# Kernel optimization log

Measured on AMD Instinct MI355X. Metric: run time of the kernel, lower is better.

## Reference

```python
import jax, jax.numpy as jnp
import numpy as np

N_Q, N_T, D, C = 4096, 8192, 512, 16
SIGMA = 2.0


def setup_inputs() -> dict:
    key = jax.random.key(0)
    k1, k2, k3 = jax.random.split(key, 3)
    X = jax.random.normal(k1, (N_Q, D), dtype=jnp.float32)
    X_train = jax.random.normal(k2, (N_T, D), dtype=jnp.float32)
    y = jax.random.randint(k3, (N_T,), 0, C, dtype=jnp.int32)
    sigma = jnp.float32(SIGMA)
    return {"X": X, "X_train": X_train, "y": y, "sigma": sigma}


def reference(X, X_train, y, sigma):
    xx = jnp.sum(X * X, axis=1, keepdims=True)              # [N_q, 1]
    tt = jnp.sum(X_train * X_train, axis=1)                 # [N_t]
    cross = jnp.einsum('qd,td->qt', X, X_train)             # [N_q, N_t]
    dist2 = jnp.maximum(xx + tt[None, :] - 2.0 * cross, 0.0)
    pattern = jnp.exp(-dist2 / (2.0 * sigma ** 2))          # Gaussian RBF kernel [N_q, N_t]
    # per-class segment sum over training patterns (replaces per-class Python loop)
    summation = jax.ops.segment_sum(pattern.T, y, num_segments=C).T  # [N_q, C]
    summation = summation / jnp.sum(summation, axis=1, keepdims=True)
    return jnp.argmax(summation, axis=1)
```

## Files before the change

kernel.cpp:

```cpp
#include <hip/hip_runtime.h>


#define NQ 4096
#define NT 8192
#define DD 512
#define NC 16
#define BM 256
#define BN 256
#define BK 64
#define NKT (DD / BK)
#define LN_FLT_MIN -87.336544750402f
#define SCREEN_T 706.0f

typedef __attribute__((ext_vector_type(8))) short bf16x8;
typedef __attribute__((ext_vector_type(4))) float f32x4;
typedef __attribute__((ext_vector_type(8))) unsigned short u16x8;

static __device__ __forceinline__ unsigned short f2bf(float f) {
  unsigned u = __float_as_uint(f);
  u = u + 0x7FFFu + ((u >> 16) & 1u);
  return (unsigned short)(u >> 16);
}

__global__ __launch_bounds__(256) void prep_k(const float* __restrict__ X,
                                              const float* __restrict__ XT,
                                              unsigned short* __restrict__ bX,
                                              unsigned short* __restrict__ bT,
                                              float* __restrict__ xx,
                                              float* __restrict__ tt,
                                              float* __restrict__ classacc) {
  const int lane = threadIdx.x & 63;
  const int row  = blockIdx.x * 4 + (threadIdx.x >> 6);
  const float* src; unsigned short* dst; float* nrm;
  if (row < NT) { src = XT + (size_t)row * DD; dst = bT + (size_t)row * DD; nrm = tt + row; }
  else { const int r = row - NT; src = X + (size_t)r * DD; dst = bX + (size_t)r * DD; nrm = xx + r; }
  const float4* s4 = (const float4*)src;
  const float4 a = s4[lane * 2], b = s4[lane * 2 + 1];
  u16x8 o;
  o[0] = f2bf(a.x); o[1] = f2bf(a.y); o[2] = f2bf(a.z); o[3] = f2bf(a.w);
  o[4] = f2bf(b.x); o[5] = f2bf(b.y); o[6] = f2bf(b.z); o[7] = f2bf(b.w);
  *((u16x8*)dst + lane) = o;
  float acc = a.x*a.x + a.y*a.y + a.z*a.z + a.w*a.w
            + b.x*b.x + b.y*b.y + b.z*b.z + b.w*b.w;
  #pragma unroll
  for (int off = 32; off; off >>= 1) acc += __shfl_down(acc, off, 64);
  if (lane == 0) *nrm = acc;
  if (blockIdx.x < 64) {
    float4 z = {0.f, 0.f, 0.f, 0.f};
    ((float4*)classacc)[blockIdx.x * 256 + threadIdx.x] = z;
  }
}

static __device__ __forceinline__ void stage_unit(const unsigned short* __restrict__ src,
                                                  int rowbase, int colbyte,
                                                  char* unitbase, int tid) {
  #pragma unroll
  for (int i = 0; i < 2; ++i) {
    const int row = i * 128 + (tid >> 2);
    const int sl  = (tid & 3) ^ ((row >> 1) & 3);
    const char* gp = (const char*)(src + (size_t)(rowbase + row) * DD) + colbyte + sl * 16;
    __builtin_amdgcn_global_load_lds(
        (const __attribute__((address_space(1))) unsigned int*)gp,
        (__attribute__((address_space(3))) unsigned int*)(unitbase + i * 8192 + (tid >> 6) * 1024),
        16, 0, 0);
  }
}

#define BAR() __builtin_amdgcn_s_barrier()

__global__ __launch_bounds__(512, 2) void pnn_mfma(const unsigned short* __restrict__ bX,
                                                   const unsigned short* __restrict__ bT,
                                                   const float* __restrict__ Xf,
                                                   const float* __restrict__ Tf,
                                                   const int* __restrict__ y,
                                                   const float* __restrict__ sigp,
                                                   const float* __restrict__ xx,
                                                   const float* __restrict__ tt,
                                                   float* __restrict__ classacc) {
  extern __shared__ char lds[];
  const int tid  = threadIdx.x;
  const int w    = tid >> 6, lane = tid & 63;
  const int wr   = w >> 2, wc = w & 3;
  const int lo   = lane & 15, hi = lane >> 4;

  const int bid = blockIdx.x;
  const int xcd = bid & 7, c = bid >> 3;
  const int qt = (xcd & 1) * 8 + (c >> 3);
  const int tn = (xcd >> 1) * 8 + (c & 7);
  const int qbase = qt * BM, tbase = tn * BN;

  char* const A0 = lds;
  char* const A1 = lds + 32768;
  char* const B0 = lds + 65536;
  char* const B1 = lds + 98304;

  const int sfix = (hi ^ ((lo >> 1) & 3)) * 16;
  const int aoff = (wr * 128 + lo) * 64 + sfix;
  const int boff = (wc * 64 + lo) * 64 + sfix;

  stage_unit(bX, qbase, 0,  A0,         tid);
  stage_unit(bT, tbase, 0,  B0,         tid);
  stage_unit(bX, qbase, 64, A0 + 16384, tid);
  stage_unit(bT, tbase, 64, B0 + 16384, tid);
  asm volatile("s_waitcnt vmcnt(4)" ::: "memory");
  __builtin_amdgcn_sched_barrier(0);
  BAR();

  f32x4 acc[8][4];
  #pragma unroll
  for (int m = 0; m < 8; ++m)
    #pragma unroll
    for (int n = 0; n < 4; ++n) acc[m][n] = (f32x4)(0.0f);

  char* Ac = A0; char* Bc = B0; char* An = A1; char* Bn = B1;

  for (int kt = 0; kt < NKT; ++kt) {
    const bool more = (kt < NKT - 1);
    const int nk = (kt + 1) * 128;
    bf16x8 a[8], b0, b1;

    #pragma unroll
    for (int m = 0; m < 8; ++m) a[m] = *(const bf16x8*)(Ac + m * 1024 + aoff);
    b0 = *(const bf16x8*)(Bc + 0 * 1024 + boff);
    b1 = *(const bf16x8*)(Bc + 1 * 1024 + boff);
    if (more) stage_unit(bX, qbase, nk, An, tid);
    BAR();
    __builtin_amdgcn_s_setprio(1);
    #pragma unroll
    for (int m = 0; m < 8; ++m) {
      acc[m][0] = __builtin_amdgcn_mfma_f32_16x16x32_bf16(a[m], b0, acc[m][0], 0, 0, 0);
      acc[m][1] = __builtin_amdgcn_mfma_f32_16x16x32_bf16(a[m], b1, acc[m][1], 0, 0, 0);
    }
    __builtin_amdgcn_s_setprio(0);
    BAR();

    b0 = *(const bf16x8*)(Bc + 2 * 1024 + boff);
    b1 = *(const bf16x8*)(Bc + 3 * 1024 + boff);
    if (more) stage_unit(bT, tbase, nk, Bn, tid);
    BAR();
    __builtin_amdgcn_s_setprio(1);
    #pragma unroll
    for (int m = 0; m < 8; ++m) {
      acc[m][2] = __builtin_amdgcn_mfma_f32_16x16x32_bf16(a[m], b0, acc[m][2], 0, 0, 0);
      acc[m][3] = __builtin_amdgcn_mfma_f32_16x16x32_bf16(a[m], b1, acc[m][3], 0, 0, 0);
    }
    __builtin_amdgcn_s_setprio(0);
    if (more) asm volatile("s_waitcnt vmcnt(4)" ::: "memory");
    else      asm volatile("s_waitcnt vmcnt(0)" ::: "memory");
    BAR();

    #pragma unroll
    for (int m = 0; m < 8; ++m) a[m] = *(const bf16x8*)(Ac + 16384 + m * 1024 + aoff);
    b0 = *(const bf16x8*)(Bc + 16384 + 0 * 1024 + boff);
    b1 = *(const bf16x8*)(Bc + 16384 + 1 * 1024 + boff);
    if (more) stage_unit(bX, qbase, nk + 64, An + 16384, tid);
    BAR();
    __builtin_amdgcn_s_setprio(1);
    #pragma unroll
    for (int m = 0; m < 8; ++m) {
      acc[m][0] = __builtin_amdgcn_mfma_f32_16x16x32_bf16(a[m], b0, acc[m][0], 0, 0, 0);
      acc[m][1] = __builtin_amdgcn_mfma_f32_16x16x32_bf16(a[m], b1, acc[m][1], 0, 0, 0);
    }
    __builtin_amdgcn_s_setprio(0);
    BAR();

    b0 = *(const bf16x8*)(Bc + 16384 + 2 * 1024 + boff);
    b1 = *(const bf16x8*)(Bc + 16384 + 3 * 1024 + boff);
    if (more) stage_unit(bT, tbase, nk + 64, Bn + 16384, tid);
    BAR();
    __builtin_amdgcn_s_setprio(1);
    #pragma unroll
    for (int m = 0; m < 8; ++m) {
      acc[m][2] = __builtin_amdgcn_mfma_f32_16x16x32_bf16(a[m], b0, acc[m][2], 0, 0, 0);
      acc[m][3] = __builtin_amdgcn_mfma_f32_16x16x32_bf16(a[m], b1, acc[m][3], 0, 0, 0);
    }
    __builtin_amdgcn_s_setprio(0);
    if (more) asm volatile("s_waitcnt vmcnt(4)" ::: "memory");
    BAR();

    char* t0 = Ac; Ac = An; An = t0;
    char* t1 = Bc; Bc = Bn; Bn = t1;
  }

  const float sg = sigp[0];
  const float inv2s2 = 1.0f / (2.0f * sg * sg);
  const int qb = qbase + wr * 128;
  const int tb = tbase + wc * 64;
  float tnorm[4]; int tcls[4];
  #pragma unroll
  for (int n = 0; n < 4; ++n) {
    const int t = tb + n * 16 + lo;
    tnorm[n] = tt[t]; tcls[n] = y[t];
  }
  #pragma unroll
  for (int m = 0; m < 8; ++m) {
    #pragma unroll
    for (int r = 0; r < 4; ++r) {
      const int q = qb + m * 16 + hi * 4 + r;
      const float xq = xx[q];
      #pragma unroll
      for (int n = 0; n < 4; ++n) {
        const float d2 = xq + tnorm[n] - 2.0f * acc[m][n][r];
        if (__builtin_expect(d2 < SCREEN_T, 0)) {
          const int t = tb + n * 16 + lo;
          const float* xp = Xf + (size_t)q * DD;
          const float* tp = Tf + (size_t)t * DD;
          float dot = 0.f;
          for (int d = 0; d < DD; ++d) dot = fmaf(xp[d], tp[d], dot);
          const float dd2 = fmaxf(xx[q] + tt[t] - 2.0f * dot, 0.f);
          const float arg = -dd2 * inv2s2;
          if (arg >= LN_FLT_MIN)
            atomicAdd(&classacc[q * NC + tcls[n]], expf(arg));
        }
      }
    }
  }
}

__global__ __launch_bounds__(256) void argmax_k(const float* __restrict__ classacc,
                                                float* __restrict__ out) {
  const int q = blockIdx.x * 256 + threadIdx.x;
  float sc[NC];
  #pragma unroll
  for (int c4 = 0; c4 < 4; ++c4) {
    const float4 v = ((const float4*)(classacc + (size_t)q * NC))[c4];
    sc[c4*4+0] = v.x; sc[c4*4+1] = v.y; sc[c4*4+2] = v.z; sc[c4*4+3] = v.w;
  }
  float rowsum = 0.f;
  #pragma unroll
  for (int c = 0; c < NC; ++c) rowsum += sc[c];
  int best = 0; float bv = sc[0];
  #pragma unroll
  for (int c = 1; c < NC; ++c)
    if (sc[c] > bv) { bv = sc[c]; best = c; }
  out[q] = (rowsum > 0.f) ? (float)best : 0.0f;
}

extern "C" void kernel_launch(void* const* d_in, const int* in_sizes, int n_in,
                              void* d_out, int out_size, void* d_ws, size_t ws_size,
                              hipStream_t stream) {
  const float* X  = (const float*)d_in[0];
  const float* XT = (const float*)d_in[1];
  const int*   y  = (const int*)d_in[2];
  const float* sg = (const float*)d_in[3];
  float* out = (float*)d_out;

  char* wsp = (char*)d_ws;
  unsigned short* bX = (unsigned short*)wsp;
  unsigned short* bT = bX + (size_t)NQ * DD;
  float* tt       = (float*)(wsp + 12u * 1024u * 1024u);
  float* xx       = tt + NT;
  float* classacc = xx + NQ;

  (void)hipFuncSetAttribute((const void*)pnn_mfma,
                            hipFuncAttributeMaxDynamicSharedMemorySize, 131072);

  prep_k<<<(NQ + NT) / 4, 256, 0, stream>>>(X, XT, bX, bT, xx, tt, classacc);
  pnn_mfma<<<512, 512, 131072, stream>>>(bX, bT, X, XT, y, sg, xx, tt, classacc);
  argmax_k<<<NQ / 256, 256, 0, stream>>>(classacc, out);
}
```

Before: 53.61 us.

## Switch screening GEMM from bf16 to fp8 with 32x32x64 scaled MFMA

Inputs are now converted to fp8 (e4m3) instead of bf16, and the screening GEMM uses the 32x32x64 f8f6f4 scaled MFMA with a reworked LDS read pattern and a three-stage prefetch schedule. This halves operand bytes and doubles MFMA throughput per instruction, targeting the GEMM phase. The coarser precision forces a looser screening threshold, so more pairs may hit the exact fp32 recompute path. That path is also vectorized to float4 with four partial sums.

After: 47.02 us. -12.3%, faster.

```diff
diff --git a/kernel.cpp b/kernel.cpp
--- a/kernel.cpp
+++ b/kernel.cpp
@@ -5,41 +5,33 @@
 #define NT 8192
 #define DD 512
 #define NC 16
-#define BM 256
-#define BN 256
-#define BK 64
-#define NKT (DD / BK)
 #define LN_FLT_MIN -87.336544750402f
-#define SCREEN_T 706.0f
-
-typedef __attribute__((ext_vector_type(8))) short bf16x8;
-typedef __attribute__((ext_vector_type(4))) float f32x4;
-typedef __attribute__((ext_vector_type(8))) unsigned short u16x8;
-
-static __device__ __forceinline__ unsigned short f2bf(float f) {
-  unsigned u = __float_as_uint(f);
-  u = u + 0x7FFFu + ((u >> 16) & 1u);
-  return (unsigned short)(u >> 16);
-}
+#define SCREEN_T 730.0f
+
+typedef __attribute__((ext_vector_type(4))) int   v4i;
+typedef __attribute__((ext_vector_type(8))) int   v8i;
+typedef __attribute__((ext_vector_type(16))) float f32x16;
 
 __global__ __launch_bounds__(256) void prep_k(const float* __restrict__ X,
                                               const float* __restrict__ XT,
-                                              unsigned short* __restrict__ bX,
-                                              unsigned short* __restrict__ bT,
+                                              unsigned char* __restrict__ fX,
+                                              unsigned char* __restrict__ fT,
                                               float* __restrict__ xx,
                                               float* __restrict__ tt,
                                               float* __restrict__ classacc) {
   const int lane = threadIdx.x & 63;
   const int row  = blockIdx.x * 4 + (threadIdx.x >> 6);
-  const float* src; unsigned short* dst; float* nrm;
-  if (row < NT) { src = XT + (size_t)row * DD; dst = bT + (size_t)row * DD; nrm = tt + row; }
-  else { const int r = row - NT; src = X + (size_t)r * DD; dst = bX + (size_t)r * DD; nrm = xx + r; }
+  const float* src; unsigned char* dst; float* nrm;
+  if (row < NT) { src = XT + (size_t)row * DD; dst = fT + (size_t)row * DD; nrm = tt + row; }
+  else { const int r = row - NT; src = X + (size_t)r * DD; dst = fX + (size_t)r * DD; nrm = xx + r; }
   const float4* s4 = (const float4*)src;
   const float4 a = s4[lane * 2], b = s4[lane * 2 + 1];
-  u16x8 o;
-  o[0] = f2bf(a.x); o[1] = f2bf(a.y); o[2] = f2bf(a.z); o[3] = f2bf(a.w);
-  o[4] = f2bf(b.x); o[5] = f2bf(b.y); o[6] = f2bf(b.z); o[7] = f2bf(b.w);
-  *((u16x8*)dst + lane) = o;
+  int w0 = __builtin_amdgcn_cvt_pk_fp8_f32(a.x, a.y, 0, false);
+  w0     = __builtin_amdgcn_cvt_pk_fp8_f32(a.z, a.w, w0, true);
+  int w1 = __builtin_amdgcn_cvt_pk_fp8_f32(b.x, b.y, 0, false);
+  w1     = __builtin_amdgcn_cvt_pk_fp8_f32(b.z, b.w, w1, true);
+  int2 o; o.x = w0; o.y = w1;
+  *(int2*)(dst + lane * 8) = o;
   float acc = a.x*a.x + a.y*a.y + a.z*a.z + a.w*a.w
             + b.x*b.x + b.y*b.y + b.z*b.z + b.w*b.w;
   #pragma unroll
@@ -51,14 +43,14 @@
   }
 }
 
-static __device__ __forceinline__ void stage_unit(const unsigned short* __restrict__ src,
+static __device__ __forceinline__ void stage_unit(const unsigned char* __restrict__ src,
                                                   int rowbase, int colbyte,
                                                   char* unitbase, int tid) {
   #pragma unroll
   for (int i = 0; i < 2; ++i) {
     const int row = i * 128 + (tid >> 2);
     const int sl  = (tid & 3) ^ ((row >> 1) & 3);
-    const char* gp = (const char*)(src + (size_t)(rowbase + row) * DD) + colbyte + sl * 16;
+    const unsigned char* gp = src + (size_t)(rowbase + row) * DD + colbyte + sl * 16;
     __builtin_amdgcn_global_load_lds(
         (const __attribute__((address_space(1))) unsigned int*)gp,
         (__attribute__((address_space(3))) unsigned int*)(unitbase + i * 8192 + (tid >> 6) * 1024),
@@ -66,10 +58,17 @@
   }
 }
 
+static __device__ __forceinline__ v8i read32(const char* base, int off) {
+  v4i lo = *(const v4i*)(base + off);
+  v4i hi = *(const v4i*)(base + (off ^ 16));
+  return __builtin_shufflevector(lo, hi, 0, 1, 2, 3, 4, 5, 6, 7);
+}
+
 #define BAR() __builtin_amdgcn_s_barrier()
-
-__global__ __launch_bounds__(512, 2) void pnn_mfma(const unsigned short* __restrict__ bX,
-                                                   const unsigned short* __restrict__ bT,
+#define WAITV(N) asm volatile("s_waitcnt vmcnt(" #N ")" ::: "memory")
+
+__global__ __launch_bounds__(512, 2) void pnn_mfma(const unsigned char* __restrict__ fX,
+                                                   const unsigned char* __restrict__ fT,
                                                    const float* __restrict__ Xf,
                                                    const float* __restrict__ Tf,
                                                    const int* __restrict__ y,
@@ -81,136 +80,111 @@
   const int tid  = threadIdx.x;
   const int w    = tid >> 6, lane = tid & 63;
   const int wr   = w >> 2, wc = w & 3;
-  const int lo   = lane & 15, hi = lane >> 4;
+  const int la   = lane & 31, lb = lane >> 5;
 
   const int bid = blockIdx.x;
   const int xcd = bid & 7, c = bid >> 3;
   const int qt = (xcd & 1) * 8 + (c >> 3);
   const int tn = (xcd >> 1) * 8 + (c & 7);
-  const int qbase = qt * BM, tbase = tn * BN;
+  const int qbase = qt * 256, tbase = tn * 256;
 
   char* const A0 = lds;
   char* const A1 = lds + 32768;
   char* const B0 = lds + 65536;
   char* const B1 = lds + 98304;
 
-  const int sfix = (hi ^ ((lo >> 1) & 3)) * 16;
-  const int aoff = (wr * 128 + lo) * 64 + sfix;
-  const int boff = (wc * 64 + lo) * 64 + sfix;
-
-  stage_unit(bX, qbase, 0,  A0,         tid);
-  stage_unit(bT, tbase, 0,  B0,         tid);
-  stage_unit(bX, qbase, 64, A0 + 16384, tid);
-  stage_unit(bT, tbase, 64, B0 + 16384, tid);
-  asm volatile("s_waitcnt vmcnt(4)" ::: "memory");
+  const int g   = (la >> 1) & 3;
+  const int p0  = (((lb * 2) ^ g) * 16);
+  const int arow = (wr * 128 + la) * 64;
+  const int brow = (wc * 64 + la) * 64;
+
+  stage_unit(fX, qbase, 0,   A0,         tid);
+  stage_unit(fT, tbase, 0,   B0,         tid);
+  stage_unit(fX, qbase, 64,  A0 + 16384, tid);
+  stage_unit(fT, tbase, 64,  B0 + 16384, tid);
+  stage_unit(fX, qbase, 128, A1,         tid);
+  stage_unit(fT, tbase, 128, B1,         tid);
+  WAITV(8);
   __builtin_amdgcn_sched_barrier(0);
   BAR();
 
-  f32x4 acc[8][4];
-  #pragma unroll
-  for (int m = 0; m < 8; ++m)
+  f32x16 acc[4][2];
+  #pragma unroll
+  for (int mt = 0; mt < 4; ++mt)
     #pragma unroll
-    for (int n = 0; n < 4; ++n) acc[m][n] = (f32x4)(0.0f);
-
-  char* Ac = A0; char* Bc = B0; char* An = A1; char* Bn = B1;
-
-  for (int kt = 0; kt < NKT; ++kt) {
-    const bool more = (kt < NKT - 1);
-    const int nk = (kt + 1) * 128;
-    bf16x8 a[8], b0, b1;
-
-    #pragma unroll
-    for (int m = 0; m < 8; ++m) a[m] = *(const bf16x8*)(Ac + m * 1024 + aoff);
-    b0 = *(const bf16x8*)(Bc + 0 * 1024 + boff);
-    b1 = *(const bf16x8*)(Bc + 1 * 1024 + boff);
-    if (more) stage_unit(bX, qbase, nk, An, tid);
-    BAR();
-    __builtin_amdgcn_s_setprio(1);
-    #pragma unroll
-    for (int m = 0; m < 8; ++m) {
-      acc[m][0] = __builtin_amdgcn_mfma_f32_16x16x32_bf16(a[m], b0, acc[m][0], 0, 0, 0);
-      acc[m][1] = __builtin_amdgcn_mfma_f32_16x16x32_bf16(a[m], b1, acc[m][1], 0, 0, 0);
-    }
-    __builtin_amdgcn_s_setprio(0);
-    BAR();
-
-    b0 = *(const bf16x8*)(Bc + 2 * 1024 + boff);
-    b1 = *(const bf16x8*)(Bc + 3 * 1024 + boff);
-    if (more) stage_unit(bT, tbase, nk, Bn, tid);
-    BAR();
-    __builtin_amdgcn_s_setprio(1);
-    #pragma unroll
-    for (int m = 0; m < 8; ++m) {
-      acc[m][2] = __builtin_amdgcn_mfma_f32_16x16x32_bf16(a[m], b0, acc[m][2], 0, 0, 0);
-      acc[m][3] = __builtin_amdgcn_mfma_f32_16x16x32_bf16(a[m], b1, acc[m][3], 0, 0, 0);
-    }
-    __builtin_amdgcn_s_setprio(0);
-    if (more) asm volatile("s_waitcnt vmcnt(4)" ::: "memory");
-    else      asm volatile("s_waitcnt vmcnt(0)" ::: "memory");
-    BAR();
-
-    #pragma unroll
-    for (int m = 0; m < 8; ++m) a[m] = *(const bf16x8*)(Ac + 16384 + m * 1024 + aoff);
-    b0 = *(const bf16x8*)(Bc + 16384 + 0 * 1024 + boff);
-    b1 = *(const bf16x8*)(Bc + 16384 + 1 * 1024 + boff);
-    if (more) stage_unit(bX, qbase, nk + 64, An + 16384, tid);
-    BAR();
-    __builtin_amdgcn_s_setprio(1);
-    #pragma unroll
-    for (int m = 0; m < 8; ++m) {
-      acc[m][0] = __builtin_amdgcn_mfma_f32_16x16x32_bf16(a[m], b0, acc[m][0], 0, 0, 0);
-      acc[m][1] = __builtin_amdgcn_mfma_f32_16x16x32_bf16(a[m], b1, acc[m][1], 0, 0, 0);
-    }
-    __builtin_amdgcn_s_setprio(0);
-    BAR();
-
-    b0 = *(const bf16x8*)(Bc + 16384 + 2 * 1024 + boff);
-    b1 = *(const bf16x8*)(Bc + 16384 + 3 * 1024 + boff);
-    if (more) stage_unit(bT, tbase, nk + 64, Bn + 16384, tid);
-    BAR();
-    __builtin_amdgcn_s_setprio(1);
-    #pragma unroll
-    for (int m = 0; m < 8; ++m) {
-      acc[m][2] = __builtin_amdgcn_mfma_f32_16x16x32_bf16(a[m], b0, acc[m][2], 0, 0, 0);
-      acc[m][3] = __builtin_amdgcn_mfma_f32_16x16x32_bf16(a[m], b1, acc[m][3], 0, 0, 0);
-    }
-    __builtin_amdgcn_s_setprio(0);
-    if (more) asm volatile("s_waitcnt vmcnt(4)" ::: "memory");
-    BAR();
-
-    char* t0 = Ac; Ac = An; An = t0;
-    char* t1 = Bc; Bc = Bn; Bn = t1;
-  }
+    for (int nt = 0; nt < 2; ++nt) acc[mt][nt] = (f32x16)(0.0f);
+
+  char* cA = A0; char* cB = B0; char* nA = A1; char* nB = B1;
+
+#define PHASE(ABASE, BBASE, STAGE_STMT, WAIT_STMT)                             \
+  {                                                                            \
+    v8i af[4], bfr[2];                                                         \
+    _Pragma("unroll")                                                          \
+    for (int mt = 0; mt < 4; ++mt) af[mt] = read32((ABASE), arow + mt * 2048 + p0); \
+    _Pragma("unroll")                                                          \
+    for (int nt = 0; nt < 2; ++nt) bfr[nt] = read32((BBASE), brow + nt * 2048 + p0); \
+    STAGE_STMT                                                                 \
+    BAR();                                                                     \
+    __builtin_amdgcn_s_setprio(1);                                             \
+    _Pragma("unroll")                                                          \
+    for (int mt = 0; mt < 4; ++mt)                                             \
+      _Pragma("unroll")                                                        \
+      for (int nt = 0; nt < 2; ++nt)                                           \
+        acc[mt][nt] = __builtin_amdgcn_mfma_scale_f32_32x32x64_f8f6f4(         \
+            af[mt], bfr[nt], acc[mt][nt], 0, 0, 0, 127, 0, 127);               \
+    __builtin_amdgcn_s_setprio(0);                                             \
+    WAIT_STMT                                                                  \
+    BAR();                                                                     \
+  }
+
+  for (int kt = 0; kt < 4; ++kt) {
+    PHASE(cA, cB,
+          { if (kt < 3) { stage_unit(fX, qbase, (2 * kt + 3) * 64, nA + 16384, tid);
+                          stage_unit(fT, tbase, (2 * kt + 3) * 64, nB + 16384, tid); } },
+          { if (kt < 3) { WAITV(8); } else { WAITV(0); } })
+    PHASE(cA + 16384, cB + 16384,
+          { if (kt < 2) { stage_unit(fX, qbase, (2 * kt + 4) * 64, cA, tid);
+                          stage_unit(fT, tbase, (2 * kt + 4) * 64, cB, tid); } },
+          { if (kt < 2) { WAITV(8); } else if (kt == 2) { WAITV(4); } })
+    char* t0 = cA; cA = nA; nA = t0;
+    char* t1 = cB; cB = nB; nB = t1;
+  }
+#undef PHASE
 
   const float sg = sigp[0];
   const float inv2s2 = 1.0f / (2.0f * sg * sg);
   const int qb = qbase + wr * 128;
-  const int tb = tbase + wc * 64;
-  float tnorm[4]; int tcls[4];
-  #pragma unroll
-  for (int n = 0; n < 4; ++n) {
-    const int t = tb + n * 16 + lo;
-    tnorm[n] = tt[t]; tcls[n] = y[t];
-  }
-  #pragma unroll
-  for (int m = 0; m < 8; ++m) {
+  const int tbc = tbase + wc * 64;
+  float tnorm[2]; int tcls[2];
+  #pragma unroll
+  for (int nt = 0; nt < 2; ++nt) {
+    const int t = tbc + nt * 32 + la;
+    tnorm[nt] = tt[t]; tcls[nt] = y[t];
+  }
+  #pragma unroll
+  for (int mt = 0; mt < 4; ++mt) {
     #pragma unroll
-    for (int r = 0; r < 4; ++r) {
-      const int q = qb + m * 16 + hi * 4 + r;
+    for (int reg = 0; reg < 16; ++reg) {
+      const int q = qb + mt * 32 + (reg & 3) + 8 * (reg >> 2) + 4 * lb;
       const float xq = xx[q];
       #pragma unroll
-      for (int n = 0; n < 4; ++n) {
-        const float d2 = xq + tnorm[n] - 2.0f * acc[m][n][r];
+      for (int nt = 0; nt < 2; ++nt) {
+        const float d2 = xq + tnorm[nt] - 2.0f * acc[mt][nt][reg];
         if (__builtin_expect(d2 < SCREEN_T, 0)) {
-          const int t = tb + n * 16 + lo;
-          const float* xp = Xf + (size_t)q * DD;
-          const float* tp = Tf + (size_t)t * DD;
-          float dot = 0.f;
-          for (int d = 0; d < DD; ++d) dot = fmaf(xp[d], tp[d], dot);
-          const float dd2 = fmaxf(xx[q] + tt[t] - 2.0f * dot, 0.f);
+          const int t = tbc + nt * 32 + la;
+          const float4* xp = (const float4*)(Xf + (size_t)q * DD);
+          const float4* tp = (const float4*)(Tf + (size_t)t * DD);
+          float s0 = 0.f, s1 = 0.f, s2 = 0.f, s3 = 0.f;
+          for (int d = 0; d < DD / 4; ++d) {
+            const float4 xv = xp[d], tv = tp[d];
+            s0 = fmaf(xv.x, tv.x, s0); s1 = fmaf(xv.y, tv.y, s1);
+            s2 = fmaf(xv.z, tv.z, s2); s3 = fmaf(xv.w, tv.w, s3);
+          }
+          const float dot = (s0 + s1) + (s2 + s3);
+          const float dd2 = fmaxf(xq + tnorm[nt] - 2.0f * dot, 0.f);
           const float arg = -dd2 * inv2s2;
           if (arg >= LN_FLT_MIN)
-            atomicAdd(&classacc[q * NC + tcls[n]], expf(arg));
+            atomicAdd(&classacc[q * NC + tcls[nt]], expf(arg));
         }
       }
     }
@@ -246,16 +220,16 @@
   float* out = (float*)d_out;
 
   char* wsp = (char*)d_ws;
-  unsigned short* bX = (unsigned short*)wsp;
-  unsigned short* bT = bX + (size_t)NQ * DD;
-  float* tt       = (float*)(wsp + 12u * 1024u * 1024u);
+  unsigned char* fX = (unsigned char*)wsp;
+  unsigned char* fT = fX + (size_t)NQ * DD;
+  float* tt       = (float*)(wsp + 8u * 1024u * 1024u);
   float* xx       = tt + NT;
   float* classacc = xx + NQ;
 
   (void)hipFuncSetAttribute((const void*)pnn_mfma,
                             hipFuncAttributeMaxDynamicSharedMemorySize, 131072);
 
-  prep_k<<<(NQ + NT) / 4, 256, 0, stream>>>(X, XT, bX, bT, xx, tt, classacc);
-  pnn_mfma<<<512, 512, 131072, stream>>>(bX, bT, X, XT, y, sg, xx, tt, classacc);
+  prep_k<<<(NQ + NT) / 4, 256, 0, stream>>>(X, XT, fX, fT, xx, tt, classacc);
+  pnn_mfma<<<512, 512, 131072, stream>>>(fX, fT, X, XT, y, sg, xx, tt, classacc);
   argmax_k<<<NQ / 256, 256, 0, stream>>>(classacc, out);
 }
```

## Restructure GEMM main loop into 4-slot ring with 3-deep prefetch

Applied to the files above, without the earlier changes.

Replaces the double-buffered K=128 pipeline with a 4-slot LDS ring of K=32 tiles, prefetching three steps ahead and using a single barrier per step. Block-to-tile mapping changes so each XCD covers a different set of training tiles. The screening test is folded into a precomputed half-norm comparison kept in LDS, and the fallback exact dot product is vectorised with float4 and four accumulators. LDS use grows slightly past 128KB, which allows only one block per CU compared with the two requested by the old launch bounds.

After: 46.88 us. 12.6% less time.

```diff
diff --git a/kernel.cpp b/kernel.cpp
--- a/kernel.cpp
+++ b/kernel.cpp
@@ -5,10 +5,6 @@
 #define NT 8192
 #define DD 512
 #define NC 16
-#define BM 256
-#define BN 256
-#define BK 64
-#define NKT (DD / BK)
 #define LN_FLT_MIN -87.336544750402f
 #define SCREEN_T 706.0f
 
@@ -51,166 +47,130 @@
   }
 }
 
+#define BAR() __builtin_amdgcn_s_barrier()
+#define WAITV(N) asm volatile("s_waitcnt vmcnt(" #N ")" ::: "memory")
+
+static __device__ __forceinline__ void gll(const void* src, char* dst) {
+  __builtin_amdgcn_global_load_lds(
+      (const __attribute__((address_space(1))) unsigned int*)src,
+      (__attribute__((address_space(3))) unsigned int*)dst, 16, 0, 0);
+}
+
 static __device__ __forceinline__ void stage_unit(const unsigned short* __restrict__ src,
-                                                  int rowbase, int colbyte,
-                                                  char* unitbase, int tid) {
-  #pragma unroll
-  for (int i = 0; i < 2; ++i) {
-    const int row = i * 128 + (tid >> 2);
-    const int sl  = (tid & 3) ^ ((row >> 1) & 3);
-    const char* gp = (const char*)(src + (size_t)(rowbase + row) * DD) + colbyte + sl * 16;
-    __builtin_amdgcn_global_load_lds(
-        (const __attribute__((address_space(1))) unsigned int*)gp,
-        (__attribute__((address_space(3))) unsigned int*)(unitbase + i * 8192 + (tid >> 6) * 1024),
-        16, 0, 0);
-  }
-}
-
-#define BAR() __builtin_amdgcn_s_barrier()
-
-__global__ __launch_bounds__(512, 2) void pnn_mfma(const unsigned short* __restrict__ bX,
-                                                   const unsigned short* __restrict__ bT,
-                                                   const float* __restrict__ Xf,
-                                                   const float* __restrict__ Tf,
-                                                   const int* __restrict__ y,
-                                                   const float* __restrict__ sigp,
-                                                   const float* __restrict__ xx,
-                                                   const float* __restrict__ tt,
-                                                   float* __restrict__ classacc) {
+                                                  int rowbase, int kt,
+                                                  char* dst, int tid) {
+  #pragma unroll
+  for (int j = 0; j < 2; ++j) {
+    const int L = j * 8192 + tid * 16;
+    const int r = L >> 6, c = L & 63;
+    const int cs = c ^ (((r >> 1) & 3) << 4);
+    gll((const char*)(src + (size_t)(rowbase + r) * DD) + kt * 64 + cs, dst + L);
+  }
+}
+
+static __device__ __forceinline__ bf16x8 frag(const char* slot, int row, int hi) {
+  const int c = (hi * 16) ^ (((row >> 1) & 3) << 4);
+  return *(const bf16x8*)(slot + row * 64 + c);
+}
+
+__global__ __launch_bounds__(512) void pnn_mfma(const unsigned short* __restrict__ bX,
+                                                const unsigned short* __restrict__ bT,
+                                                const float* __restrict__ Xf,
+                                                const float* __restrict__ Tf,
+                                                const int* __restrict__ y,
+                                                const float* __restrict__ sigp,
+                                                const float* __restrict__ xx,
+                                                const float* __restrict__ tt,
+                                                float* __restrict__ classacc) {
   extern __shared__ char lds[];
+  float* const hxs = (float*)(lds + 131072);
   const int tid  = threadIdx.x;
   const int w    = tid >> 6, lane = tid & 63;
+  const int lo   = lane & 15, hb = lane >> 4;
   const int wr   = w >> 2, wc = w & 3;
-  const int lo   = lane & 15, hi = lane >> 4;
 
   const int bid = blockIdx.x;
   const int xcd = bid & 7, c = bid >> 3;
-  const int qt = (xcd & 1) * 8 + (c >> 3);
-  const int tn = (xcd >> 1) * 8 + (c & 7);
-  const int qbase = qt * BM, tbase = tn * BN;
-
-  char* const A0 = lds;
-  char* const A1 = lds + 32768;
-  char* const B0 = lds + 65536;
-  char* const B1 = lds + 98304;
-
-  const int sfix = (hi ^ ((lo >> 1) & 3)) * 16;
-  const int aoff = (wr * 128 + lo) * 64 + sfix;
-  const int boff = (wc * 64 + lo) * 64 + sfix;
-
-  stage_unit(bX, qbase, 0,  A0,         tid);
-  stage_unit(bT, tbase, 0,  B0,         tid);
-  stage_unit(bX, qbase, 64, A0 + 16384, tid);
-  stage_unit(bT, tbase, 64, B0 + 16384, tid);
-  asm volatile("s_waitcnt vmcnt(4)" ::: "memory");
-  __builtin_amdgcn_sched_barrier(0);
-  BAR();
+  const int tn  = xcd * 4 + (c & 3);
+  const int qt  = c >> 2;
+  const int qbase = qt * 256, tbase = tn * 256;
+
+#define ASLOT(k) (lds + ((k) & 3) * 16384)
+#define BSLOT(k) (lds + 65536 + ((k) & 3) * 16384)
+
+  float xv = 0.f;
+  if (tid < 256) xv = xx[qbase + tid];
+  stage_unit(bX, qbase, 0, ASLOT(0), tid);
+  stage_unit(bT, tbase, 0, BSLOT(0), tid);
+  stage_unit(bX, qbase, 1, ASLOT(1), tid);
+  stage_unit(bT, tbase, 1, BSLOT(1), tid);
+  stage_unit(bX, qbase, 2, ASLOT(2), tid);
+  stage_unit(bT, tbase, 2, BSLOT(2), tid);
+  if (tid < 256) hxs[tid] = (xv - SCREEN_T) * 0.5f;
 
   f32x4 acc[8][4];
   #pragma unroll
   for (int m = 0; m < 8; ++m)
     #pragma unroll
-    for (int n = 0; n < 4; ++n) acc[m][n] = (f32x4)(0.0f);
-
-  char* Ac = A0; char* Bc = B0; char* An = A1; char* Bn = B1;
-
-  for (int kt = 0; kt < NKT; ++kt) {
-    const bool more = (kt < NKT - 1);
-    const int nk = (kt + 1) * 128;
-    bf16x8 a[8], b0, b1;
-
-    #pragma unroll
-    for (int m = 0; m < 8; ++m) a[m] = *(const bf16x8*)(Ac + m * 1024 + aoff);
-    b0 = *(const bf16x8*)(Bc + 0 * 1024 + boff);
-    b1 = *(const bf16x8*)(Bc + 1 * 1024 + boff);
-    if (more) stage_unit(bX, qbase, nk, An, tid);
+    for (int n = 0; n < 4; ++n) acc[m][n] = (f32x4)(0.f);
+
+  #pragma unroll
+  for (int k = 0; k < 16; ++k) {
+    if (k <= 13) { WAITV(8); } else if (k == 14) { WAITV(4); } else { WAITV(0); }
+    __builtin_amdgcn_sched_barrier(0);
     BAR();
-    __builtin_amdgcn_s_setprio(1);
-    #pragma unroll
-    for (int m = 0; m < 8; ++m) {
-      acc[m][0] = __builtin_amdgcn_mfma_f32_16x16x32_bf16(a[m], b0, acc[m][0], 0, 0, 0);
-      acc[m][1] = __builtin_amdgcn_mfma_f32_16x16x32_bf16(a[m], b1, acc[m][1], 0, 0, 0);
-    }
-    __builtin_amdgcn_s_setprio(0);
-    BAR();
-
-    b0 = *(const bf16x8*)(Bc + 2 * 1024 + boff);
-    b1 = *(const bf16x8*)(Bc + 3 * 1024 + boff);
-    if (more) stage_unit(bT, tbase, nk, Bn, tid);
-    BAR();
-    __builtin_amdgcn_s_setprio(1);
-    #pragma unroll
-    for (int m = 0; m < 8; ++m) {
-      acc[m][2] = __builtin_amdgcn_mfma_f32_16x16x32_bf16(a[m], b0, acc[m][2], 0, 0, 0);
-      acc[m][3] = __builtin_amdgcn_mfma_f32_16x16x32_bf16(a[m], b1, acc[m][3], 0, 0, 0);
-    }
-    __builtin_amdgcn_s_setprio(0);
-    if (more) asm volatile("s_waitcnt vmcnt(4)" ::: "memory");
-    else      asm volatile("s_waitcnt vmcnt(0)" ::: "memory");
-    BAR();
-
-    #pragma unroll
-    for (int m = 0; m < 8; ++m) a[m] = *(const bf16x8*)(Ac + 16384 + m * 1024 + aoff);
-    b0 = *(const bf16x8*)(Bc + 16384 + 0 * 1024 + boff);
-    b1 = *(const bf16x8*)(Bc + 16384 + 1 * 1024 + boff);
-    if (more) stage_unit(bX, qbase, nk + 64, An + 16384, tid);
-    BAR();
-    __builtin_amdgcn_s_setprio(1);
-    #pragma unroll
-    for (int m = 0; m < 8; ++m) {
-      acc[m][0] = __builtin_amdgcn_mfma_f32_16x16x32_bf16(a[m], b0, acc[m][0], 0, 0, 0);
-      acc[m][1] = __builtin_amdgcn_mfma_f32_16x16x32_bf16(a[m], b1, acc[m][1], 0, 0, 0);
-    }
-    __builtin_amdgcn_s_setprio(0);
-    BAR();
-
-    b0 = *(const bf16x8*)(Bc + 16384 + 2 * 1024 + boff);
-    b1 = *(const bf16x8*)(Bc + 16384 + 3 * 1024 + boff);
-    if (more) stage_unit(bT, tbase, nk + 64, Bn + 16384, tid);
-    BAR();
-    __builtin_amdgcn_s_setprio(1);
-    #pragma unroll
-    for (int m = 0; m < 8; ++m) {
-      acc[m][2] = __builtin_amdgcn_mfma_f32_16x16x32_bf16(a[m], b0, acc[m][2], 0, 0, 0);
-      acc[m][3] = __builtin_amdgcn_mfma_f32_16x16x32_bf16(a[m], b1, acc[m][3], 0, 0, 0);
-    }
-    __builtin_amdgcn_s_setprio(0);
-    if (more) asm volatile("s_waitcnt vmcnt(4)" ::: "memory");
-    BAR();
-
-    char* t0 = Ac; Ac = An; An = t0;
-    char* t1 = Bc; Bc = Bn; Bn = t1;
+    const char* As = ASLOT(k);
+    const char* Bs = BSLOT(k);
+    bf16x8 bfr[4], af[4];
+    #pragma unroll
+    for (int n = 0; n < 4; ++n) bfr[n] = frag(Bs, wc * 64 + n * 16 + lo, hb);
+    #pragma unroll
+    for (int m = 0; m < 4; ++m) af[m] = frag(As, wr * 128 + m * 16 + lo, hb);
+    if (k <= 12) stage_unit(bX, qbase, k + 3, ASLOT(k + 3), tid);
+    #pragma unroll
+    for (int m = 0; m < 4; ++m)
+      #pragma unroll
+      for (int n = 0; n < 4; ++n)
+        acc[m][n] = __builtin_amdgcn_mfma_f32_16x16x32_bf16(af[m], bfr[n], acc[m][n], 0, 0, 0);
+    #pragma unroll
+    for (int m = 0; m < 4; ++m) af[m] = frag(As, wr * 128 + (m + 4) * 16 + lo, hb);
+    if (k <= 12) stage_unit(bT, tbase, k + 3, BSLOT(k + 3), tid);
+    #pragma unroll
+    for (int m = 0; m < 4; ++m)
+      #pragma unroll
+      for (int n = 0; n < 4; ++n)
+        acc[m + 4][n] = __builtin_amdgcn_mfma_f32_16x16x32_bf16(af[m], bfr[n], acc[m + 4][n], 0, 0, 0);
   }
 
   const float sg = sigp[0];
   const float inv2s2 = 1.0f / (2.0f * sg * sg);
-  const int qb = qbase + wr * 128;
-  const int tb = tbase + wc * 64;
-  float tnorm[4]; int tcls[4];
-  #pragma unroll
-  for (int n = 0; n < 4; ++n) {
-    const int t = tb + n * 16 + lo;
-    tnorm[n] = tt[t]; tcls[n] = y[t];
-  }
+  float tnorm[4];
+  #pragma unroll
+  for (int n = 0; n < 4; ++n) tnorm[n] = tt[tbase + wc * 64 + n * 16 + lo] * 0.5f;
+
   #pragma unroll
   for (int m = 0; m < 8; ++m) {
     #pragma unroll
-    for (int r = 0; r < 4; ++r) {
-      const int q = qb + m * 16 + hi * 4 + r;
-      const float xq = xx[q];
+    for (int n = 0; n < 4; ++n) {
       #pragma unroll
-      for (int n = 0; n < 4; ++n) {
-        const float d2 = xq + tnorm[n] - 2.0f * acc[m][n][r];
-        if (__builtin_expect(d2 < SCREEN_T, 0)) {
-          const int t = tb + n * 16 + lo;
-          const float* xp = Xf + (size_t)q * DD;
-          const float* tp = Tf + (size_t)t * DD;
-          float dot = 0.f;
-          for (int d = 0; d < DD; ++d) dot = fmaf(xp[d], tp[d], dot);
-          const float dd2 = fmaxf(xx[q] + tt[t] - 2.0f * dot, 0.f);
+      for (int r = 0; r < 4; ++r) {
+        const int ql = wr * 128 + m * 16 + hb * 4 + r;
+        if (__builtin_expect(acc[m][n][r] > hxs[ql] + tnorm[n], 0)) {
+          const int q = qbase + ql;
+          const int tg = tbase + wc * 64 + n * 16 + lo;
+          const float4* xp = (const float4*)(Xf + (size_t)q * DD);
+          const float4* tp = (const float4*)(Tf + (size_t)tg * DD);
+          float s0 = 0.f, s1 = 0.f, s2 = 0.f, s3 = 0.f;
+          for (int d = 0; d < DD / 4; ++d) {
+            const float4 xw = xp[d], tw = tp[d];
+            s0 = fmaf(xw.x, tw.x, s0); s1 = fmaf(xw.y, tw.y, s1);
+            s2 = fmaf(xw.z, tw.z, s2); s3 = fmaf(xw.w, tw.w, s3);
+          }
+          const float dot = (s0 + s1) + (s2 + s3);
+          const float dd2 = fmaxf(xx[q] + tt[tg] - 2.0f * dot, 0.f);
           const float arg = -dd2 * inv2s2;
           if (arg >= LN_FLT_MIN)
-            atomicAdd(&classacc[q * NC + tcls[n]], expf(arg));
+            atomicAdd(&classacc[q * NC + y[tg]], expf(arg));
         }
       }
     }
@@ -253,9 +213,9 @@
   float* classacc = xx + NQ;
 
   (void)hipFuncSetAttribute((const void*)pnn_mfma,
-                            hipFuncAttributeMaxDynamicSharedMemorySize, 131072);
+                            hipFuncAttributeMaxDynamicSharedMemorySize, 132096);
 
   prep_k<<<(NQ + NT) / 4, 256, 0, stream>>>(X, XT, bX, bT, xx, tt, classacc);
-  pnn_mfma<<<512, 512, 131072, stream>>>(bX, bT, X, XT, y, sg, xx, tt, classacc);
+  pnn_mfma<<<512, 512, 132096, stream>>>(bX, bT, X, XT, y, sg, xx, tt, classacc);
   argmax_k<<<NQ / 256, 256, 0, stream>>>(classacc, out);
 }
```
